# Performance work log

Hardware: AMD Instinct MI355X
Metric: run time of the kernel (lower is better)

The kernel has to match this reference:

```python
import jax, jax.numpy as jnp
import numpy as np

B, S, D, H = 16, 577, 1280, 16
HD = D // H  # 80
HALF = HD // 2  # 40


def setup_inputs() -> dict:
    key = jax.random.key(0)
    ks = jax.random.split(key, 8)
    hidden_states = jax.random.normal(ks[0], (B, S, D), dtype=jnp.float32)
    # 2D rotary frequencies: random angles -> unit-magnitude complex rotations
    angles = jax.random.uniform(ks[1], (S, HALF), dtype=jnp.float32) * (2.0 * np.pi)
    freqs_cos = jnp.cos(angles)
    freqs_sin = jnp.sin(angles)
    scale = 1.0 / np.sqrt(D)
    Wq = jax.random.normal(ks[2], (D, D), dtype=jnp.float32) * scale
    Wk = jax.random.normal(ks[3], (D, D), dtype=jnp.float32) * scale
    Wv = jax.random.normal(ks[4], (D, D), dtype=jnp.float32) * scale
    Wo = jax.random.normal(ks[5], (D, D), dtype=jnp.float32) * scale
    z = jnp.zeros((D,), dtype=jnp.float32)
    return {
        "hidden_states": hidden_states,
        "freqs_cos": freqs_cos,
        "freqs_sin": freqs_sin,
        "Wq": Wq, "bq": z, "Wk": Wk, "bk": z,
        "Wv": Wv, "bv": z, "Wo": Wo, "bo": z,
    }


def _apply_rotary(x, cos, sin):
    # x: [B,S,H,HD]; cos/sin: [S, HD/2]; interleaved complex pairs (even=real, odd=imag)
    xr = x[..., 0::2]
    xi = x[..., 1::2]
    c = cos[None, :, None, :]
    s = sin[None, :, None, :]
    out_r = xr * c - xi * s
    out_i = xr * s + xi * c
    # re-interleave pairs back to [..., HD]
    return jnp.stack([out_r, out_i], axis=-1).reshape(x.shape)


def reference(hidden_states, freqs_cos, freqs_sin, Wq, bq, Wk, bk, Wv, bv, Wo, bo):
    q = (hidden_states @ Wq.T + bq).reshape(B, S, H, HD)
    k = (hidden_states @ Wk.T + bk).reshape(B, S, H, HD)
    v = (hidden_states @ Wv.T + bv).reshape(B, S, H, HD)
    q = _apply_rotary(q, freqs_cos, freqs_sin)
    k = _apply_rotary(k, freqs_cos, freqs_sin)
    # [B,H,S,HD]
    q = q.transpose(0, 2, 1, 3)
    k = k.transpose(0, 2, 1, 3)
    v = v.transpose(0, 2, 1, 3)
    scale = 1.0 / np.sqrt(HD).astype(np.float32)
    scores = jnp.einsum("bhsd,bhtd->bhst", q, k) * scale
    probs = jax.nn.softmax(scores, axis=-1)
    attn = jnp.einsum("bhst,bhtd->bhsd", probs, v)
    attn = attn.transpose(0, 2, 1, 3).reshape(B, S, D)
    return attn @ Wo.T + bo
```

## Files before the change

kernel.cpp:

```cpp
#include <hip/hip_runtime.h>

#define B_N 16
#define S_N 577
#define D_N 1280
#define H_N 16
#define HD_N 80
#define HALF_N 40
#define M_N 9232
#define M_PAD 9344
#define K_N 1280
#define VT_S 608
#define QSCALE 0.11180339887498949f

typedef __bf16 bf16_t;
typedef bf16_t bf16x8 __attribute__((ext_vector_type(8)));
typedef float f32x4 __attribute__((ext_vector_type(4)));

__device__ __forceinline__ float bf2f(unsigned short u) {
    union { unsigned int i; float f; } x; x.i = ((unsigned int)u) << 16; return x.f;
}
__device__ __forceinline__ unsigned short f2bf(float f) {
    union { unsigned int i; float f; } x; x.f = f;
    unsigned int r = x.i + 0x7FFFu + ((x.i >> 16) & 1u);
    return (unsigned short)(r >> 16);
}

__device__ __forceinline__ void gld_lds16(const unsigned short* g, unsigned short* l) {
    __builtin_amdgcn_global_load_lds(
        (const __attribute__((address_space(1))) unsigned int*)g,
        (__attribute__((address_space(3))) unsigned int*)l,
        16, 0, 0);
}

__global__ __launch_bounds__(256) void cvt_kernel(const float* __restrict__ in,
                                                  unsigned short* __restrict__ out, int n4) {
    int i = blockIdx.x * 256 + threadIdx.x;
    if (i < n4) {
        float4 v = ((const float4*)in)[i];
        ushort4 o;
        o.x = f2bf(v.x); o.y = f2bf(v.y); o.z = f2bf(v.z); o.w = f2bf(v.w);
        ((ushort4*)out)[i] = o;
    }
}

#define W4_N (D_N * K_N / 4)
__global__ __launch_bounds__(256) void cvt4_kernel(
    const float* __restrict__ w0, const float* __restrict__ w1,
    const float* __restrict__ w2, const float* __restrict__ w3,
    unsigned short* __restrict__ out) {
    int i = blockIdx.x * 256 + threadIdx.x;
    if (i >= 4 * W4_N) return;
    int r = i / W4_N, j = i - r * W4_N;
    const float* src = (r == 0) ? w0 : (r == 1) ? w1 : (r == 2) ? w2 : w3;
    float4 v = ((const float4*)src)[j];
    ushort4 o;
    o.x = f2bf(v.x); o.y = f2bf(v.y); o.z = f2bf(v.z); o.w = f2bf(v.w);
    ((ushort4*)out)[i] = o;
}

template <int MODE>
__global__ __launch_bounds__(256) void mgemm_kernel(
    const unsigned short* __restrict__ A,
    const unsigned short* __restrict__ Wb,
    const float* __restrict__ bias,
    const float* __restrict__ cosb, const float* __restrict__ sinb,
    void* __restrict__ out_)
{
    __shared__ __align__(16) unsigned short As[128 * 32];
    __shared__ __align__(16) unsigned short Bs[128 * 32];

    const int tid = threadIdx.x;
    const int wave = tid >> 6, lane = tid & 63;
    const int quad = lane >> 4, n = lane & 15;
    const int wm = wave >> 1, wn = wave & 1;
    const int m0 = blockIdx.y * 128, n0 = blockIdx.x * 128;

    const int ldrow = lane >> 2;
    const int ldk = (lane & 3) * 8;

    const unsigned short* gA = A + (size_t)(m0 + wave * 32 + ldrow) * K_N + ldk;
    const unsigned short* gB = Wb + (size_t)(n0 + wave * 32 + ldrow) * K_N + ldk;
    unsigned short* lA = As + wave * 32 * 32;
    unsigned short* lB = Bs + wave * 32 * 32;

    f32x4 acc[4][4] = {};

    for (int k0 = 0; k0 < K_N; k0 += 32) {
        gld_lds16(gA + k0, lA);
        gld_lds16(gA + k0 + 16 * K_N, lA + 16 * 32);
        gld_lds16(gB + k0, lB);
        gld_lds16(gB + k0 + 16 * K_N, lB + 16 * 32);
        __syncthreads();

        bf16x8 af[4], bfr[4];
        #pragma unroll
        for (int mt = 0; mt < 4; ++mt)
            af[mt] = *(const bf16x8*)&As[(wm * 64 + mt * 16 + n) * 32 + quad * 8];
        #pragma unroll
        for (int nt = 0; nt < 4; ++nt)
            bfr[nt] = *(const bf16x8*)&Bs[(wn * 64 + nt * 16 + n) * 32 + quad * 8];
        #pragma unroll
        for (int mt = 0; mt < 4; ++mt)
            #pragma unroll
            for (int nt = 0; nt < 4; ++nt)
                acc[mt][nt] = __builtin_amdgcn_mfma_f32_16x16x32_bf16(
                    af[mt], bfr[nt], acc[mt][nt], 0, 0, 0);
        __syncthreads();
    }

    const int nbase = n0 + wn * 64;
    const int mbase = m0 + wm * 64;

    if (MODE == 3) {
        float* out = (float*)out_;
        #pragma unroll
        for (int mt = 0; mt < 4; ++mt)
            #pragma unroll
            for (int nt = 0; nt < 4; ++nt) {
                const int ncol = nbase + nt * 16 + n;
                const float bv = bias[ncol];
                #pragma unroll
                for (int r = 0; r < 4; ++r) {
                    int mrow = mbase + mt * 16 + quad * 4 + r;
                    if (mrow < M_N)
                        out[(size_t)mrow * D_N + ncol] = acc[mt][nt][r] + bv;
                }
            }
    } else {
        unsigned short* out = (unsigned short*)out_;
        const bool evn = (n & 1) == 0;
        #pragma unroll
        for (int nt = 0; nt < 4; ++nt) {
            const int ncol = nbase + nt * 16 + n;
            const int h = ncol / HD_N, hd = ncol - h * HD_N;
            const float bv = bias[ncol];
            #pragma unroll
            for (int mt = 0; mt < 4; ++mt)
                #pragma unroll
                for (int r = 0; r < 4; ++r) {
                    int mrow = mbase + mt * 16 + quad * 4 + r;
                    int b = mrow / S_N, s = mrow - b * S_N;
                    float v = acc[mt][nt][r] + bv;
                    float res;
                    if (MODE == 2) {
                        res = v;
                    } else {
                        float pv = __shfl_xor(v, 1);
                        float c  = cosb[s * HALF_N + (hd >> 1)];
                        float sn = sinb[s * HALF_N + (hd >> 1)];
                        res = evn ? (v * c - pv * sn) : (pv * sn + v * c);
                        if (MODE == 0) res *= QSCALE;
                    }
                    if (mrow < M_N) {
                        if (MODE == 2)
                            out[((size_t)(b * H_N + h) * HD_N + hd) * VT_S + s] = f2bf(res);
                        else
                            out[((size_t)(b * H_N + h) * S_N + s) * HD_N + hd] = f2bf(res);
                    }
                }
        }
    }
}

__global__ __launch_bounds__(256) void fattn_kernel(
    const unsigned short* __restrict__ qb,
    const unsigned short* __restrict__ kb,
    const unsigned short* __restrict__ vt,
    unsigned short* __restrict__ attn)
{
    __shared__ __align__(16) unsigned short Plds[4][2][2][16 * 32];

    const int tid = threadIdx.x;
    const int wave = tid >> 6, lane = tid & 63;
    const int quad = lane >> 4, n = lane & 15;

    const int bid = blockIdx.x;
    const int xcd = bid & 7, t = bid >> 3;
    const int qt = t % 5, hl = t / 5;
    const int bh = hl * 8 + xcd;
    const int q0 = qt * 128 + wave * 32;

    const bf16x8 zf{};
    const unsigned short* qrow0 = qb + ((size_t)bh * S_N + q0 + n) * HD_N;
    const unsigned short* qrow1 = qrow0 + 16 * HD_N;
    bf16x8 aq00 = *(const bf16x8*)(qrow0 + quad * 8);
    bf16x8 aq01 = *(const bf16x8*)(qrow0 + 32 + quad * 8);
    bf16x8 aq02 = (quad < 2) ? *(const bf16x8*)(qrow0 + 64 + quad * 8) : zf;
    bf16x8 aq10 = *(const bf16x8*)(qrow1 + quad * 8);
    bf16x8 aq11 = *(const bf16x8*)(qrow1 + 32 + quad * 8);
    bf16x8 aq12 = (quad < 2) ? *(const bf16x8*)(qrow1 + 64 + quad * 8) : zf;

    const bf16_t one = (bf16_t)1.0f;
    const bf16x8 vones_all = {one, one, one, one, one, one, one, one};
    const bf16x8 vones = (n == 0) ? vones_all : zf;

    f32x4 o0[6] = {};
    f32x4 o1[6] = {};

    const unsigned short* kbase = kb + (size_t)bh * S_N * HD_N;
    const unsigned short* vbase = vt + (size_t)bh * HD_N * VT_S;

    #pragma unroll 2
    for (int t0 = 0; t0 < 608; t0 += 32) {
        const int pp = (t0 >> 5) & 1;
        unsigned short* pl0 = &Plds[wave][pp][0][0];
        unsigned short* pl1 = &Plds[wave][pp][1][0];

        const unsigned short* krA = kbase + (size_t)(t0 + n) * HD_N;
        const unsigned short* krB = krA + 16 * HD_N;
        bf16x8 bA0 = *(const bf16x8*)(krA + quad * 8);
        bf16x8 bA1 = *(const bf16x8*)(krA + 32 + quad * 8);
        bf16x8 bA2 = (quad < 2) ? *(const bf16x8*)(krA + 64 + quad * 8) : zf;
        bf16x8 bB0 = *(const bf16x8*)(krB + quad * 8);
        bf16x8 bB1 = *(const bf16x8*)(krB + 32 + quad * 8);
        bf16x8 bB2 = (quad < 2) ? *(const bf16x8*)(krB + 64 + quad * 8) : zf;

        f32x4 c00{}, c01{}, c10{}, c11{};
        c00 = __builtin_amdgcn_mfma_f32_16x16x32_bf16(aq00, bA0, c00, 0, 0, 0);
        c00 = __builtin_amdgcn_mfma_f32_16x16x32_bf16(aq01, bA1, c00, 0, 0, 0);
        c00 = __builtin_amdgcn_mfma_f32_16x16x32_bf16(aq02, bA2, c00, 0, 0, 0);
        c01 = __builtin_amdgcn_mfma_f32_16x16x32_bf16(aq00, bB0, c01, 0, 0, 0);
        c01 = __builtin_amdgcn_mfma_f32_16x16x32_bf16(aq01, bB1, c01, 0, 0, 0);
        c01 = __builtin_amdgcn_mfma_f32_16x16x32_bf16(aq02, bB2, c01, 0, 0, 0);
        c10 = __builtin_amdgcn_mfma_f32_16x16x32_bf16(aq10, bA0, c10, 0, 0, 0);
        c10 = __builtin_amdgcn_mfma_f32_16x16x32_bf16(aq11, bA1, c10, 0, 0, 0);
        c10 = __builtin_amdgcn_mfma_f32_16x16x32_bf16(aq12, bA2, c10, 0, 0, 0);
        c11 = __builtin_amdgcn_mfma_f32_16x16x32_bf16(aq10, bB0, c11, 0, 0, 0);
        c11 = __builtin_amdgcn_mfma_f32_16x16x32_bf16(aq11, bB1, c11, 0, 0, 0);
        c11 = __builtin_amdgcn_mfma_f32_16x16x32_bf16(aq12, bB2, c11, 0, 0, 0);

        const bool mA = (t0 + n) >= S_N;
        const bool mB = (t0 + 16 + n) >= S_N;

        #pragma unroll
        for (int r = 0; r < 4; ++r) {
            float p00 = mA ? 0.0f : __expf(c00[r]);
            float p01 = mB ? 0.0f : __expf(c01[r]);
            float p10 = mA ? 0.0f : __expf(c10[r]);
            float p11 = mB ? 0.0f : __expf(c11[r]);
            pl0[(quad * 4 + r) * 32 + n]      = f2bf(p00);
            pl0[(quad * 4 + r) * 32 + 16 + n] = f2bf(p01);
            pl1[(quad * 4 + r) * 32 + n]      = f2bf(p10);
            pl1[(quad * 4 + r) * 32 + 16 + n] = f2bf(p11);
        }

        bf16x8 ap0 = *(const bf16x8*)(pl0 + n * 32 + quad * 8);
        bf16x8 ap1 = *(const bf16x8*)(pl1 + n * 32 + quad * 8);

        #pragma unroll
        for (int nt = 0; nt < 5; ++nt) {
            const unsigned short* vr = vbase + (size_t)(nt * 16 + n) * VT_S + t0 + quad * 8;
            bf16x8 bv = *(const bf16x8*)vr;
            o0[nt] = __builtin_amdgcn_mfma_f32_16x16x32_bf16(ap0, bv, o0[nt], 0, 0, 0);
            o1[nt] = __builtin_amdgcn_mfma_f32_16x16x32_bf16(ap1, bv, o1[nt], 0, 0, 0);
        }
        o0[5] = __builtin_amdgcn_mfma_f32_16x16x32_bf16(ap0, vones, o0[5], 0, 0, 0);
        o1[5] = __builtin_amdgcn_mfma_f32_16x16x32_bf16(ap1, vones, o1[5], 0, 0, 0);
    }

    const int b = bh >> 4, h = bh & 15;
    #pragma unroll
    for (int r = 0; r < 4; ++r) {
        float l0 = __shfl(o0[5][r], lane & 48);
        float l1 = __shfl(o1[5][r], lane & 48);
        float linv0 = 1.0f / l0, linv1 = 1.0f / l1;
        int s0 = q0 + quad * 4 + r;
        int s1 = s0 + 16;
        #pragma unroll
        for (int nt = 0; nt < 5; ++nt) {
            if (s0 < S_N)
                attn[((size_t)b * S_N + s0) * D_N + h * HD_N + nt * 16 + n] =
                    f2bf(o0[nt][r] * linv0);
            if (s1 < S_N)
                attn[((size_t)b * S_N + s1) * D_N + h * HD_N + nt * 16 + n] =
                    f2bf(o1[nt][r] * linv1);
        }
    }
}

extern "C" void kernel_launch(void* const* d_in, const int* in_sizes, int n_in,
                              void* d_out, int out_size, void* d_ws, size_t ws_size,
                              hipStream_t stream) {
    const float* hs = (const float*)d_in[0];
    const float* fc = (const float*)d_in[1];
    const float* fs = (const float*)d_in[2];
    const float* Wq = (const float*)d_in[3];
    const float* bq = (const float*)d_in[4];
    const float* Wk = (const float*)d_in[5];
    const float* bk = (const float*)d_in[6];
    const float* Wv = (const float*)d_in[7];
    const float* bv = (const float*)d_in[8];
    const float* Wo = (const float*)d_in[9];
    const float* bo = (const float*)d_in[10];
    float* out = (float*)d_out;

    char* ws = (char*)d_ws;
    size_t off = 0;
    auto alloc = [&](size_t bytes) {
        char* p = ws + off; off += (bytes + 255) & ~(size_t)255; return p;
    };
    unsigned short* hsb  = (unsigned short*)alloc((size_t)M_PAD * K_N * 2);
    unsigned short* qb   = (unsigned short*)alloc((size_t)M_N * K_N * 2 + 32768);
    unsigned short* kb   = (unsigned short*)alloc((size_t)M_N * K_N * 2 + 32768);
    unsigned short* vt   = (unsigned short*)alloc((size_t)B_N * H_N * HD_N * VT_S * 2);
    unsigned short* Wall = (unsigned short*)alloc((size_t)4 * D_N * K_N * 2);

    const int HS4 = M_N * K_N / 4;
    dim3 blk(256);
    dim3 ggrid(D_N / 128, M_PAD / 128);

    cvt_kernel<<<(HS4 + 255) / 256, blk, 0, stream>>>(hs, hsb, HS4);
    cvt4_kernel<<<(4 * W4_N + 255) / 256, blk, 0, stream>>>(Wq, Wk, Wv, Wo, Wall);

    mgemm_kernel<0><<<ggrid, blk, 0, stream>>>(
        hsb, Wall + 0 * (size_t)D_N * K_N, bq, fc, fs, qb);
    mgemm_kernel<1><<<ggrid, blk, 0, stream>>>(
        hsb, Wall + 1 * (size_t)D_N * K_N, bk, fc, fs, kb);
    mgemm_kernel<2><<<ggrid, blk, 0, stream>>>(
        hsb, Wall + 2 * (size_t)D_N * K_N, bv, fc, fs, vt);

    fattn_kernel<<<dim3(1280), blk, 0, stream>>>(qb, kb, vt, hsb );

    mgemm_kernel<3><<<ggrid, blk, 0, stream>>>(
        hsb, Wall + 3 * (size_t)D_N * K_N, bo, fc, fs, out);
}
```

Measured before the change: 502.9 us.

## Fuse QKV projections into one GEMM launch with K=64 swizzled LDS tiles

The three separate Q/K/V projection GEMMs become one launch over a 30-wide column grid. Each block picks its bias, output buffer and epilogue (rotary plus scale, rotary, or transposed V) from its column block. The GEMM K-step doubles to 64, and the LDS tiles use an XOR swizzle to avoid bank conflicts on fragment reads, which halves the number of barriers per K. The cost is twice the LDS per block and a runtime branch in the epilogue, which may lower occupancy.

```diff
diff --git a/kernel.cpp b/kernel.cpp
--- a/kernel.cpp
+++ b/kernel.cpp
@@ -59,66 +59,72 @@
 }
 
 template <int MODE>
-__global__ __launch_bounds__(256) void mgemm_kernel(
+__global__ __launch_bounds__(256) void mgemm64_kernel(
     const unsigned short* __restrict__ A,
     const unsigned short* __restrict__ Wb,
-    const float* __restrict__ bias,
+    const float* __restrict__ b0, const float* __restrict__ b1,
+    const float* __restrict__ b2,
     const float* __restrict__ cosb, const float* __restrict__ sinb,
-    void* __restrict__ out_)
+    void* __restrict__ o0, void* __restrict__ o1, void* __restrict__ o2)
 {
-    __shared__ __align__(16) unsigned short As[128 * 32];
-    __shared__ __align__(16) unsigned short Bs[128 * 32];
+    __shared__ __align__(16) unsigned short As[128 * 64];
+    __shared__ __align__(16) unsigned short Bs[128 * 64];
 
     const int tid = threadIdx.x;
     const int wave = tid >> 6, lane = tid & 63;
     const int quad = lane >> 4, n = lane & 15;
     const int wm = wave >> 1, wn = wave & 1;
-    const int m0 = blockIdx.y * 128, n0 = blockIdx.x * 128;
-
-    const int ldrow = lane >> 2;
-    const int ldk = (lane & 3) * 8;
-
-    const unsigned short* gA = A + (size_t)(m0 + wave * 32 + ldrow) * K_N + ldk;
-    const unsigned short* gB = Wb + (size_t)(n0 + wave * 32 + ldrow) * K_N + ldk;
-    unsigned short* lA = As + wave * 32 * 32;
-    unsigned short* lB = Bs + wave * 32 * 32;
+    const int m0 = blockIdx.y * 128, n0g = blockIdx.x * 128;
+
+    const int srow = lane >> 3;
+    const int scol = (((lane & 7) ^ srow) * 8);
+
+    const unsigned short* gA = A + (size_t)(m0 + wave * 32 + srow) * K_N + scol;
+    const unsigned short* gB = Wb + (size_t)(n0g + wave * 32 + srow) * K_N + scol;
+    unsigned short* lA = As + wave * 32 * 64;
+    unsigned short* lB = Bs + wave * 32 * 64;
 
     f32x4 acc[4][4] = {};
 
-    for (int k0 = 0; k0 < K_N; k0 += 32) {
-        gld_lds16(gA + k0, lA);
-        gld_lds16(gA + k0 + 16 * K_N, lA + 16 * 32);
-        gld_lds16(gB + k0, lB);
-        gld_lds16(gB + k0 + 16 * K_N, lB + 16 * 32);
+    for (int k0 = 0; k0 < K_N; k0 += 64) {
+        #pragma unroll
+        for (int i = 0; i < 4; ++i) {
+            gld_lds16(gA + k0 + i * 8 * K_N, lA + i * 512);
+            gld_lds16(gB + k0 + i * 8 * K_N, lB + i * 512);
+        }
         __syncthreads();
 
-        bf16x8 af[4], bfr[4];
-        #pragma unroll
-        for (int mt = 0; mt < 4; ++mt)
-            af[mt] = *(const bf16x8*)&As[(wm * 64 + mt * 16 + n) * 32 + quad * 8];
-        #pragma unroll
-        for (int nt = 0; nt < 4; ++nt)
-            bfr[nt] = *(const bf16x8*)&Bs[(wn * 64 + nt * 16 + n) * 32 + quad * 8];
-        #pragma unroll
-        for (int mt = 0; mt < 4; ++mt)
+        #pragma unroll
+        for (int kk = 0; kk < 2; ++kk) {
+            const int sa = ((((kk << 2) | quad) ^ (n & 7)) * 8);
+            bf16x8 af[4], bfr[4];
+            #pragma unroll
+            for (int mt = 0; mt < 4; ++mt)
+                af[mt] = *(const bf16x8*)&As[(wm * 64 + mt * 16 + n) * 64 + sa];
             #pragma unroll
             for (int nt = 0; nt < 4; ++nt)
-                acc[mt][nt] = __builtin_amdgcn_mfma_f32_16x16x32_bf16(
-                    af[mt], bfr[nt], acc[mt][nt], 0, 0, 0);
+                bfr[nt] = *(const bf16x8*)&Bs[(wn * 64 + nt * 16 + n) * 64 + sa];
+            #pragma unroll
+            for (int mt = 0; mt < 4; ++mt)
+                #pragma unroll
+                for (int nt = 0; nt < 4; ++nt)
+                    acc[mt][nt] = __builtin_amdgcn_mfma_f32_16x16x32_bf16(
+                        af[mt], bfr[nt], acc[mt][nt], 0, 0, 0);
+        }
         __syncthreads();
     }
 
-    const int nbase = n0 + wn * 64;
     const int mbase = m0 + wm * 64;
 
     if (MODE == 3) {
-        float* out = (float*)out_;
+        const int nbase = n0g + wn * 64;
+        float* out = (float*)o0;
         #pragma unroll
         for (int mt = 0; mt < 4; ++mt)
             #pragma unroll
             for (int nt = 0; nt < 4; ++nt) {
                 const int ncol = nbase + nt * 16 + n;
-                const float bv = bias[ncol];
+                const float bv = b0[ncol];
                 #pragma unroll
                 for (int r = 0; r < 4; ++r) {
                     int mrow = mbase + mt * 16 + quad * 4 + r;
@@ -127,11 +133,15 @@
                 }
             }
     } else {
-        unsigned short* out = (unsigned short*)out_;
+        const int wsel = blockIdx.x / 10;
+        const float* bias = (wsel == 0) ? b0 : (wsel == 1) ? b1 : b2;
+        unsigned short* out =
+            (unsigned short*)((wsel == 0) ? o0 : (wsel == 1) ? o1 : o2);
+        const int nloc = n0g - wsel * 1280 + wn * 64;
         const bool evn = (n & 1) == 0;
         #pragma unroll
         for (int nt = 0; nt < 4; ++nt) {
-            const int ncol = nbase + nt * 16 + n;
+            const int ncol = nloc + nt * 16 + n;
             const int h = ncol / HD_N, hd = ncol - h * HD_N;
             const float bv = bias[ncol];
             #pragma unroll
@@ -141,21 +151,19 @@
                     int mrow = mbase + mt * 16 + quad * 4 + r;
                     int b = mrow / S_N, s = mrow - b * S_N;
                     float v = acc[mt][nt][r] + bv;
-                    float res;
-                    if (MODE == 2) {
-                        res = v;
+                    if (wsel == 2) {
+                        if (mrow < M_N)
+                            out[((size_t)(b * H_N + h) * HD_N + hd) * VT_S + s] =
+                                f2bf(v);
                     } else {
                         float pv = __shfl_xor(v, 1);
                         float c  = cosb[s * HALF_N + (hd >> 1)];
                         float sn = sinb[s * HALF_N + (hd >> 1)];
-                        res = evn ? (v * c - pv * sn) : (pv * sn + v * c);
-                        if (MODE == 0) res *= QSCALE;
-                    }
-                    if (mrow < M_N) {
-                        if (MODE == 2)
-                            out[((size_t)(b * H_N + h) * HD_N + hd) * VT_S + s] = f2bf(res);
-                        else
-                            out[((size_t)(b * H_N + h) * S_N + s) * HD_N + hd] = f2bf(res);
+                        float res = evn ? (v * c - pv * sn) : (pv * sn + v * c);
+                        if (wsel == 0) res *= QSCALE;
+                        if (mrow < M_N)
+                            out[((size_t)(b * H_N + h) * S_N + s) * HD_N + hd] =
+                                f2bf(res);
                     }
                 }
         }
@@ -307,20 +315,15 @@
 
     const int HS4 = M_N * K_N / 4;
     dim3 blk(256);
-    dim3 ggrid(D_N / 128, M_PAD / 128);
 
     cvt_kernel<<<(HS4 + 255) / 256, blk, 0, stream>>>(hs, hsb, HS4);
     cvt4_kernel<<<(4 * W4_N + 255) / 256, blk, 0, stream>>>(Wq, Wk, Wv, Wo, Wall);
 
-    mgemm_kernel<0><<<ggrid, blk, 0, stream>>>(
-        hsb, Wall + 0 * (size_t)D_N * K_N, bq, fc, fs, qb);
-    mgemm_kernel<1><<<ggrid, blk, 0, stream>>>(
-        hsb, Wall + 1 * (size_t)D_N * K_N, bk, fc, fs, kb);
-    mgemm_kernel<2><<<ggrid, blk, 0, stream>>>(
-        hsb, Wall + 2 * (size_t)D_N * K_N, bv, fc, fs, vt);
+    mgemm64_kernel<4><<<dim3(30, 73), blk, 0, stream>>>(
+        hsb, Wall, bq, bk, bv, fc, fs, qb, kb, vt);
 
     fattn_kernel<<<dim3(1280), blk, 0, stream>>>(qb, kb, vt, hsb );
 
-    mgemm_kernel<3><<<ggrid, blk, 0, stream>>>(
-        hsb, Wall + 3 * (size_t)D_N * K_N, bo, fc, fs, out);
-}
+    mgemm64_kernel<3><<<dim3(10, 73), blk, 0, stream>>>(
+        hsb, Wall + 3 * (size_t)D_N * K_N, bo, bo, bo, fc, fs, out, out, out);
+}
```

New measurement: 458.3 us. -8.9%, faster.
